# Kernel tuning notes

Measured on AMD Instinct MI355X. Metric: run time of the kernel, lower is better.

## Reference

```python
import jax, jax.numpy as jnp
import numpy as np

SCALE = 2
GROUPS = 4

def _up_axis(x, axis, s):
    # torch F.interpolate bilinear, align_corners=False, along one axis
    n = x.shape[axis]
    src = jnp.maximum((jnp.arange(n * s, dtype=jnp.float32) + 0.5) / s - 0.5, 0.0)
    i0 = jnp.minimum(jnp.floor(src).astype(jnp.int32), n - 1)
    i1 = jnp.minimum(i0 + 1, n - 1)
    t = (src - i0.astype(jnp.float32)).astype(x.dtype)
    shp = [1] * x.ndim
    shp[axis] = -1
    t = t.reshape(shp)
    return jnp.take(x, i0, axis=axis) * (1 - t) + jnp.take(x, i1, axis=axis) * t

def _grid_sample(img, grid):
    # img: (N,C,H,W); grid: (N,Hg,Wg,2) xy in [-1,1]; bilinear, align_corners=False, zeros padding
    N, C, H, W = img.shape
    gx = (grid[..., 0] + 1.0) * (W * 0.5) - 0.5
    gy = (grid[..., 1] + 1.0) * (H * 0.5) - 0.5
    x0 = jnp.floor(gx)
    y0 = jnp.floor(gy)
    tx = (gx - x0).astype(img.dtype)
    ty = (gy - y0).astype(img.dtype)
    x0 = x0.astype(jnp.int32)
    y0 = y0.astype(jnp.int32)
    flat = img.reshape(N, C, H * W)

    def corner(xi, yi, wgt):
        valid = ((xi >= 0) & (xi < W) & (yi >= 0) & (yi < H)).astype(img.dtype)
        idx = (jnp.clip(yi, 0, H - 1) * W + jnp.clip(xi, 0, W - 1)).reshape(N, -1)
        v = jax.vmap(lambda f, i: f[:, i])(flat, idx)  # (N,C,P) irregular gather
        return v * (wgt * valid).reshape(N, 1, -1)

    out = (corner(x0, y0, (1 - tx) * (1 - ty))
           + corner(x0 + 1, y0, tx * (1 - ty))
           + corner(x0, y0 + 1, (1 - tx) * ty)
           + corner(x0 + 1, y0 + 1, tx * ty))
    return out.reshape(N, C, grid.shape[1], grid.shape[2])

def _forward(x, w_off, b_off, w_mask, b_mask):
    s, g = SCALE, GROUPS
    b, c, h, w = x.shape
    # 1x1 convs
    offset = jnp.einsum('bchw,oc->bohw', x, w_off) + b_off[None, :, None, None]  # (b,2g,h,w)
    mask = jax.nn.sigmoid(jnp.einsum('bchw,gc->bghw', x, w_mask) + b_mask[None, :, None, None])  # (b,g,h,w)
    # bilinear upsample then split into s*s subpixel feature maps (one per group)
    x_up = _up_axis(_up_axis(x, 2, s), 3, s)  # (b,c,s*h,s*w)
    feat = x_up.reshape(b, c, s, h, s, w).transpose(0, 2, 4, 1, 3, 5).reshape(b, s * s, c, h, w)[:, :g]
    # per-group offset-perturbed sampling coordinates
    off = offset.reshape(b, g, 2, h, w).transpose(0, 1, 3, 4, 2)  # (b,g,h,w,2) (x,y)
    gy, gx = jnp.meshgrid(jnp.arange(h, dtype=x.dtype), jnp.arange(w, dtype=x.dtype), indexing='ij')
    base = jnp.stack([gx, gy], axis=-1)  # (h,w,2)
    coords = base[None, None] + off
    norm = (coords / jnp.array([w, h], dtype=x.dtype) - 0.5) * 2.0
    sampled = _grid_sample(feat.reshape(b * g, c, h, w), norm.reshape(b * g, h, w, 2))
    sampled = sampled.reshape(b, g, c, h, w)
    # sigmoid-mask weighting and group-sum reduction
    return (sampled * mask[:, :, None]).sum(axis=1)  # (b,c,h,w)

def setup_inputs():
    key = jax.random.key(0)
    k1, k2, k3, k4, k5 = jax.random.split(key, 5)
    b, c, h, w, g = 16, 64, 128, 128, GROUPS
    return {
        'x': jax.random.normal(k1, (b, c, h, w), jnp.float32),
        'w_off': jax.random.normal(k2, (2 * g, c), jnp.float32) * 0.1,
        'b_off': jax.random.normal(k3, (2 * g,), jnp.float32) * 0.1,
        'w_mask': jax.random.normal(k4, (g, c), jnp.float32) * 0.1,
        'b_mask': jax.random.normal(k5, (g,), jnp.float32) * 0.1,
    }

def reference(x, w_off, b_off, w_mask, b_mask):
    return _forward(x, w_off, b_off, w_mask, b_mask)
```

## Files before the change

kernel.cpp:

```cpp
#include <hip/hip_runtime.h>
#include <hip/hip_fp16.h>

#define CC 64
#define HH 128
#define WW 128
#define HWS (HH * WW)
#define NG 4

__device__ __forceinline__ void make_taps(float gp, int n, int half, int& base,
                                          float& w0o, float& w1o, float& w2o) {
  float w0 = 0.0f, w1 = 0.0f, w2 = 0.0f;
  float f = floorf(gp);
  int x0 = (int)f;
  float t = gp - f;
  int b = 0;
#pragma unroll
  for (int k = 0; k < 2; ++k) {
    int xc = x0 + k;
    float cw = k ? t : 1.0f - t;
    if (xc < 0 || xc >= n) cw = 0.0f;
    int xcc = min(max(xc, 0), n - 1);
    int u = half * n + xcc;
    float src = fmaxf((float)u * 0.5f - 0.25f, 0.0f);
    float sf = floorf(src);
    int i0 = (int)sf;
    float tu = src - sf;
    int i1 = min(i0 + 1, n - 1);
    if (k == 0) b = i0;
    int s0 = i0 - b;
    int s1 = i1 - b;
    float a0 = cw * (1.0f - tu);
    float a1 = cw * tu;
    w0 += (s0 == 0) ? a0 : 0.0f;
    w1 += (s0 == 1) ? a0 : 0.0f;
    w0 += (s1 == 0) ? a1 : 0.0f;
    w1 += (s1 == 1) ? a1 : 0.0f;
    w2 += (s1 == 2) ? a1 : 0.0f;
  }
  base = b;
  w0o = w0; w1o = w1; w2o = w2;
}

__global__ __launch_bounds__(256) void prep_fused(
    const float* __restrict__ x,
    const float* __restrict__ w_off, const float* __restrict__ b_off,
    const float* __restrict__ w_mask, const float* __restrict__ b_mask,
    __half* __restrict__ xT, float* __restrict__ geomC, int npix) {
  __shared__ float wt[CC * 12];
  int t = threadIdx.x;
  for (int idx = t; idx < CC * 12; idx += 256) {
    int c = idx / 12, d = idx - c * 12;
    wt[idx] = (d < 8) ? w_off[d * CC + c] : w_mask[(d - 8) * CC + c];
  }
  __syncthreads();

  int pix = blockIdx.x * 256 + t;
  int b = pix >> 14;
  int ij = pix & (HWS - 1);
  int i = ij >> 7, j = ij & (WW - 1);
  const float* __restrict__ xp = x + (size_t)b * CC * HWS + ij;
  __half* __restrict__ xto = xT + (size_t)pix * 64;

  float a12[12];
#pragma unroll
  for (int d = 0; d < 12; ++d) a12[d] = (d < 8) ? b_off[d] : b_mask[d - 8];

  for (int c0 = 0; c0 < CC; c0 += 8) {
    float xv[8];
#pragma unroll
    for (int k = 0; k < 8; ++k) xv[k] = xp[(size_t)(c0 + k) * HWS];
#pragma unroll
    for (int k = 0; k < 8; ++k) {
      int c = c0 + k;
      float v = xv[k];
      const float4 w0 = *reinterpret_cast<const float4*>(&wt[c * 12 + 0]);
      const float4 w1 = *reinterpret_cast<const float4*>(&wt[c * 12 + 4]);
      const float4 w2 = *reinterpret_cast<const float4*>(&wt[c * 12 + 8]);
      a12[0]  = fmaf(w0.x, v, a12[0]);   a12[1]  = fmaf(w0.y, v, a12[1]);
      a12[2]  = fmaf(w0.z, v, a12[2]);   a12[3]  = fmaf(w0.w, v, a12[3]);
      a12[4]  = fmaf(w1.x, v, a12[4]);   a12[5]  = fmaf(w1.y, v, a12[5]);
      a12[6]  = fmaf(w1.z, v, a12[6]);   a12[7]  = fmaf(w1.w, v, a12[7]);
      a12[8]  = fmaf(w2.x, v, a12[8]);   a12[9]  = fmaf(w2.y, v, a12[9]);
      a12[10] = fmaf(w2.z, v, a12[10]);  a12[11] = fmaf(w2.w, v, a12[11]);
    }
    uint4 u;
    u.x = __builtin_bit_cast(unsigned int, __floats2half2_rn(xv[0], xv[1]));
    u.y = __builtin_bit_cast(unsigned int, __floats2half2_rn(xv[2], xv[3]));
    u.z = __builtin_bit_cast(unsigned int, __floats2half2_rn(xv[4], xv[5]));
    u.w = __builtin_bit_cast(unsigned int, __floats2half2_rn(xv[6], xv[7]));
    *reinterpret_cast<uint4*>(xto + c0) = u;
  }

  float* __restrict__ gb = geomC + (size_t)(pix >> 5) * 1024 + (pix & 31);
#pragma unroll
  for (int g = 0; g < NG; ++g) {
    int sy = g >> 1, sx = g & 1;
    float mg = 1.0f / (1.0f + __expf(-a12[8 + g]));
    int cb, rb;
    float x0, x1, x2, y0, y1, y2;
    make_taps((float)j + a12[2 * g]     - 0.5f, WW, sx, cb, x0, x1, x2);
    make_taps((float)i + a12[2 * g + 1] - 0.5f, HH, sy, rb, y0, y1, y2);
    gb[(g * 8 + 0) * 32] = x0;
    gb[(g * 8 + 1) * 32] = x1;
    gb[(g * 8 + 2) * 32] = x2;
    gb[(g * 8 + 3) * 32] = y0 * mg;
    gb[(g * 8 + 4) * 32] = y1 * mg;
    gb[(g * 8 + 5) * 32] = y2 * mg;
    gb[(g * 8 + 6) * 32] = __int_as_float(rb);
    gb[(g * 8 + 7) * 32] = __int_as_float(cb);
  }
}

__global__ __launch_bounds__(256) void sample16(
    const __half* __restrict__ xT, const float* __restrict__ geomC,
    float* __restrict__ out, int npix) {
  __shared__ float graw[1024];
  __shared__ int2 gexp[32][36];
  int t = threadIdx.x;

  int nwg = gridDim.x, bid = blockIdx.x;
  int swz = ((nwg & 7) == 0) ? ((bid & 7) * (nwg >> 3) + (bid >> 3)) : bid;

  reinterpret_cast<uint4*>(graw)[t] =
      reinterpret_cast<const uint4*>(geomC + (size_t)swz * 1024)[t];
  __syncthreads();

  if (t < 128) {
    int p = t >> 2, g = t & 3;
    float wx0 = graw[(g * 8 + 0) * 32 + p];
    float wx1 = graw[(g * 8 + 1) * 32 + p];
    float wx2 = graw[(g * 8 + 2) * 32 + p];
    float wy0 = graw[(g * 8 + 3) * 32 + p];
    float wy1 = graw[(g * 8 + 4) * 32 + p];
    float wy2 = graw[(g * 8 + 5) * 32 + p];
    int rb = __float_as_int(graw[(g * 8 + 6) * 32 + p]);
    int cb = __float_as_int(graw[(g * 8 + 7) * 32 + p]);
#pragma unroll
    for (int dy = 0; dy < 3; ++dy) {
      int ro = min(rb + dy, HH - 1) * WW;
      float wyv = (dy == 0) ? wy0 : ((dy == 1) ? wy1 : wy2);
#pragma unroll
      for (int dx = 0; dx < 3; ++dx) {
        int off = ro + min(cb + dx, WW - 1);
        float wv = wyv * ((dx == 0) ? wx0 : ((dx == 1) ? wx1 : wx2));
        gexp[p][g * 9 + dy * 3 + dx] = make_int2(off, __float_as_int(wv));
      }
    }
  }
  __syncthreads();

  int p = t >> 3, r = t & 7;
  int pix = swz * 32 + p;
  int b = pix >> 14, ij = pix & (HWS - 1);
  const __half* __restrict__ xb = xT + ((size_t)b * HWS) * 64 + r * 8;

  float acc[8];
#pragma unroll
  for (int c = 0; c < 8; ++c) acc[c] = 0.0f;

#pragma unroll
  for (int k = 0; k < 36; ++k) {
    int2 ow = gexp[p][k];
    float w = __int_as_float(ow.y);
    uint4 v = *reinterpret_cast<const uint4*>(xb + (size_t)ow.x * 64);
    float2 f0 = __half22float2(__builtin_bit_cast(__half2, v.x));
    float2 f1 = __half22float2(__builtin_bit_cast(__half2, v.y));
    float2 f2 = __half22float2(__builtin_bit_cast(__half2, v.z));
    float2 f3 = __half22float2(__builtin_bit_cast(__half2, v.w));
    acc[0] = fmaf(w, f0.x, acc[0]);  acc[1] = fmaf(w, f0.y, acc[1]);
    acc[2] = fmaf(w, f1.x, acc[2]);  acc[3] = fmaf(w, f1.y, acc[3]);
    acc[4] = fmaf(w, f2.x, acc[4]);  acc[5] = fmaf(w, f2.y, acc[5]);
    acc[6] = fmaf(w, f3.x, acc[6]);  acc[7] = fmaf(w, f3.y, acc[7]);
  }

  float* __restrict__ op = out + ((size_t)b * CC + r * 8) * HWS + ij;
#pragma unroll
  for (int c = 0; c < 8; ++c) op[(size_t)c * HWS] = acc[c];
}

__global__ __launch_bounds__(256) void dysample_fused(
    const float* __restrict__ x,
    const float* __restrict__ w_off, const float* __restrict__ b_off,
    const float* __restrict__ w_mask, const float* __restrict__ b_mask,
    float* __restrict__ out, int npix) {
  __shared__ float wt[CC * 12];
  for (int idx = threadIdx.x; idx < CC * 12; idx += 256) {
    int c = idx / 12, d = idx - c * 12;
    wt[idx] = (d < 8) ? w_off[d * CC + c] : w_mask[(d - 8) * CC + c];
  }
  __syncthreads();
  int nwg = gridDim.x;
  int bid = blockIdx.x;
  int swz = ((nwg & 7) == 0) ? ((bid & 7) * (nwg >> 3) + (bid >> 3)) : bid;
  int pix = swz * 256 + threadIdx.x;
  if (pix >= npix) return;
  int b = pix >> 14;
  int ij = pix & (HWS - 1);
  int i = ij >> 7, j = ij & (WW - 1);
  const float* __restrict__ xp = x + (size_t)b * CC * HWS;
  float a12[12];
#pragma unroll
  for (int d = 0; d < 12; ++d) a12[d] = (d < 8) ? b_off[d] : b_mask[d - 8];
#pragma unroll 4
  for (int c = 0; c < CC; ++c) {
    float xv = xp[c * HWS + ij];
    const float4 w0 = *reinterpret_cast<const float4*>(&wt[c * 12 + 0]);
    const float4 w1 = *reinterpret_cast<const float4*>(&wt[c * 12 + 4]);
    const float4 w2 = *reinterpret_cast<const float4*>(&wt[c * 12 + 8]);
    a12[0]  = fmaf(w0.x, xv, a12[0]);   a12[1]  = fmaf(w0.y, xv, a12[1]);
    a12[2]  = fmaf(w0.z, xv, a12[2]);   a12[3]  = fmaf(w0.w, xv, a12[3]);
    a12[4]  = fmaf(w1.x, xv, a12[4]);   a12[5]  = fmaf(w1.y, xv, a12[5]);
    a12[6]  = fmaf(w1.z, xv, a12[6]);   a12[7]  = fmaf(w1.w, xv, a12[7]);
    a12[8]  = fmaf(w2.x, xv, a12[8]);   a12[9]  = fmaf(w2.y, xv, a12[9]);
    a12[10] = fmaf(w2.z, xv, a12[10]);  a12[11] = fmaf(w2.w, xv, a12[11]);
  }
  int ro[NG][3], co[NG][3];
  float wx[NG][3], wy[NG][3];
#pragma unroll
  for (int g = 0; g < NG; ++g) {
    int sy = g >> 1, sx = g & 1;
    float mg = 1.0f / (1.0f + __expf(-a12[8 + g]));
    int cb, rb;
    float x0, x1, x2, y0, y1, y2;
    make_taps((float)j + a12[2 * g]     - 0.5f, WW, sx, cb, x0, x1, x2);
    make_taps((float)i + a12[2 * g + 1] - 0.5f, HH, sy, rb, y0, y1, y2);
    wx[g][0] = x0;      wx[g][1] = x1;      wx[g][2] = x2;
    wy[g][0] = y0 * mg; wy[g][1] = y1 * mg; wy[g][2] = y2 * mg;
#pragma unroll
    for (int d = 0; d < 3; ++d) {
      ro[g][d] = min(rb + d, HH - 1) * WW;
      co[g][d] = min(cb + d, WW - 1);
    }
  }
  float* __restrict__ op = out + (size_t)b * CC * HWS + ij;
  for (int blk = 0; blk < 4; ++blk) {
    const float* __restrict__ xb = xp + blk * 16 * HWS;
    float acc[16];
#pragma unroll
    for (int c = 0; c < 16; ++c) acc[c] = 0.0f;
#pragma unroll
    for (int g = 0; g < NG; ++g) {
      int o9[9];
      float w9[9];
#pragma unroll
      for (int dy = 0; dy < 3; ++dy) {
#pragma unroll
        for (int dx = 0; dx < 3; ++dx) {
          o9[dy * 3 + dx] = ro[g][dy] + co[g][dx];
          w9[dy * 3 + dx] = wy[g][dy] * wx[g][dx];
        }
      }
#pragma unroll
      for (int c = 0; c < 16; ++c) {
        const float* __restrict__ xc = xb + c * HWS;
#pragma unroll
        for (int k = 0; k < 9; ++k) acc[c] = fmaf(w9[k], xc[o9[k]], acc[c]);
      }
    }
#pragma unroll
    for (int c = 0; c < 16; ++c) op[(blk * 16 + c) * HWS] = acc[c];
  }
}

extern "C" void kernel_launch(void* const* d_in, const int* in_sizes, int n_in,
                              void* d_out, int out_size, void* d_ws, size_t ws_size,
                              hipStream_t stream) {
  const float* x      = (const float*)d_in[0];
  const float* w_off  = (const float*)d_in[1];
  const float* b_off  = (const float*)d_in[2];
  const float* w_mask = (const float*)d_in[3];
  const float* b_mask = (const float*)d_in[4];
  float* out = (float*)d_out;

  int B = in_sizes[0] / (CC * HWS);
  int npix = B * HWS;
  size_t need = (size_t)npix * 128 + (size_t)npix * 128;

  if (ws_size >= need && (npix & 255) == 0) {
    __half* xT   = (__half*)d_ws;
    float* geomC = (float*)((char*)d_ws + (size_t)npix * 128);
    hipLaunchKernelGGL(prep_fused, dim3(npix / 256), dim3(256), 0, stream,
                       x, w_off, b_off, w_mask, b_mask, xT, geomC, npix);
    hipLaunchKernelGGL(sample16, dim3(npix / 32), dim3(256), 0, stream,
                       xT, geomC, out, npix);
  } else {
    int nblk = (npix + 255) / 256;
    hipLaunchKernelGGL(dysample_fused, dim3(nblk), dim3(256), 0, stream,
                       x, w_off, b_off, w_mask, b_mask, out, npix);
  }
}
```

Baseline: 99.11 us.

## Split prep channels across threads with LDS transpose; accumulate sampling in packed half2

The prep kernel now assigns each block 64 pixels, with four threads per pixel each handling 16 channels. Partial 1x1-conv sums are reduced through shared memory, and the fp16 channels-last tile is written with coalesced 16-byte stores through an LDS transpose. The sampling kernel packs weights as half2 and accumulates with packed half2 FMAs instead of fp32 FMAs after conversion. This is meant to cut conversion and ALU cost and to raise memory parallelism in prep, but accumulating 36 taps in fp16 can lose accuracy.

After: 82.63 us. -16.6%, faster.

```diff
diff --git a/kernel.cpp b/kernel.cpp
--- a/kernel.cpp
+++ b/kernel.cpp
@@ -41,12 +41,14 @@
   w0o = w0; w1o = w1; w2o = w2;
 }
 
-__global__ __launch_bounds__(256) void prep_fused(
+__global__ __launch_bounds__(256) void prep_v3(
     const float* __restrict__ x,
     const float* __restrict__ w_off, const float* __restrict__ b_off,
     const float* __restrict__ w_mask, const float* __restrict__ b_mask,
     __half* __restrict__ xT, float* __restrict__ geomC, int npix) {
   __shared__ float wt[CC * 12];
+  __shared__ unsigned int tile[64][33];
+  __shared__ float part[4][64][13];
   int t = threadIdx.x;
   for (int idx = t; idx < CC * 12; idx += 256) {
     int c = idx / 12, d = idx - c * 12;
@@ -54,60 +56,84 @@
   }
   __syncthreads();
 
-  int pix = blockIdx.x * 256 + t;
+  int px = t & 63, chq = t >> 6;
+  int pix = blockIdx.x * 64 + px;
   int b = pix >> 14;
   int ij = pix & (HWS - 1);
-  int i = ij >> 7, j = ij & (WW - 1);
   const float* __restrict__ xp = x + (size_t)b * CC * HWS + ij;
-  __half* __restrict__ xto = xT + (size_t)pix * 64;
-
-  float a12[12];
-#pragma unroll
-  for (int d = 0; d < 12; ++d) a12[d] = (d < 8) ? b_off[d] : b_mask[d - 8];
-
-  for (int c0 = 0; c0 < CC; c0 += 8) {
-    float xv[8];
-#pragma unroll
-    for (int k = 0; k < 8; ++k) xv[k] = xp[(size_t)(c0 + k) * HWS];
-#pragma unroll
-    for (int k = 0; k < 8; ++k) {
-      int c = c0 + k;
-      float v = xv[k];
-      const float4 w0 = *reinterpret_cast<const float4*>(&wt[c * 12 + 0]);
-      const float4 w1 = *reinterpret_cast<const float4*>(&wt[c * 12 + 4]);
-      const float4 w2 = *reinterpret_cast<const float4*>(&wt[c * 12 + 8]);
-      a12[0]  = fmaf(w0.x, v, a12[0]);   a12[1]  = fmaf(w0.y, v, a12[1]);
-      a12[2]  = fmaf(w0.z, v, a12[2]);   a12[3]  = fmaf(w0.w, v, a12[3]);
-      a12[4]  = fmaf(w1.x, v, a12[4]);   a12[5]  = fmaf(w1.y, v, a12[5]);
-      a12[6]  = fmaf(w1.z, v, a12[6]);   a12[7]  = fmaf(w1.w, v, a12[7]);
-      a12[8]  = fmaf(w2.x, v, a12[8]);   a12[9]  = fmaf(w2.y, v, a12[9]);
-      a12[10] = fmaf(w2.z, v, a12[10]);  a12[11] = fmaf(w2.w, v, a12[11]);
-    }
-    uint4 u;
-    u.x = __builtin_bit_cast(unsigned int, __floats2half2_rn(xv[0], xv[1]));
-    u.y = __builtin_bit_cast(unsigned int, __floats2half2_rn(xv[2], xv[3]));
-    u.z = __builtin_bit_cast(unsigned int, __floats2half2_rn(xv[4], xv[5]));
-    u.w = __builtin_bit_cast(unsigned int, __floats2half2_rn(xv[6], xv[7]));
-    *reinterpret_cast<uint4*>(xto + c0) = u;
-  }
-
-  float* __restrict__ gb = geomC + (size_t)(pix >> 5) * 1024 + (pix & 31);
-#pragma unroll
-  for (int g = 0; g < NG; ++g) {
-    int sy = g >> 1, sx = g & 1;
-    float mg = 1.0f / (1.0f + __expf(-a12[8 + g]));
-    int cb, rb;
-    float x0, x1, x2, y0, y1, y2;
-    make_taps((float)j + a12[2 * g]     - 0.5f, WW, sx, cb, x0, x1, x2);
-    make_taps((float)i + a12[2 * g + 1] - 0.5f, HH, sy, rb, y0, y1, y2);
-    gb[(g * 8 + 0) * 32] = x0;
-    gb[(g * 8 + 1) * 32] = x1;
-    gb[(g * 8 + 2) * 32] = x2;
-    gb[(g * 8 + 3) * 32] = y0 * mg;
-    gb[(g * 8 + 4) * 32] = y1 * mg;
-    gb[(g * 8 + 5) * 32] = y2 * mg;
-    gb[(g * 8 + 6) * 32] = __int_as_float(rb);
-    gb[(g * 8 + 7) * 32] = __int_as_float(cb);
+
+  float xv[16];
+#pragma unroll
+  for (int k = 0; k < 16; ++k) xv[k] = xp[(size_t)(chq * 16 + k) * HWS];
+
+  float p12[12];
+#pragma unroll
+  for (int d = 0; d < 12; ++d) p12[d] = 0.0f;
+#pragma unroll
+  for (int k = 0; k < 16; ++k) {
+    int c = chq * 16 + k;
+    float v = xv[k];
+    const float4 w0 = *reinterpret_cast<const float4*>(&wt[c * 12 + 0]);
+    const float4 w1 = *reinterpret_cast<const float4*>(&wt[c * 12 + 4]);
+    const float4 w2 = *reinterpret_cast<const float4*>(&wt[c * 12 + 8]);
+    p12[0]  = fmaf(w0.x, v, p12[0]);   p12[1]  = fmaf(w0.y, v, p12[1]);
+    p12[2]  = fmaf(w0.z, v, p12[2]);   p12[3]  = fmaf(w0.w, v, p12[3]);
+    p12[4]  = fmaf(w1.x, v, p12[4]);   p12[5]  = fmaf(w1.y, v, p12[5]);
+    p12[6]  = fmaf(w1.z, v, p12[6]);   p12[7]  = fmaf(w1.w, v, p12[7]);
+    p12[8]  = fmaf(w2.x, v, p12[8]);   p12[9]  = fmaf(w2.y, v, p12[9]);
+    p12[10] = fmaf(w2.z, v, p12[10]);  p12[11] = fmaf(w2.w, v, p12[11]);
+  }
+
+#pragma unroll
+  for (int k = 0; k < 8; ++k) {
+    tile[px][chq * 8 + k] = __builtin_bit_cast(
+        unsigned int, __floats2half2_rn(xv[2 * k], xv[2 * k + 1]));
+  }
+#pragma unroll
+  for (int d = 0; d < 12; ++d) part[chq][px][d] = p12[d];
+  __syncthreads();
+
+  {
+    unsigned int* __restrict__ xtu = reinterpret_cast<unsigned int*>(xT);
+    size_t base = (size_t)blockIdx.x * 64 * 32;
+    int spx = t >> 2, c0 = (t & 3) * 8;
+    uint4 u0, u1;
+    u0.x = tile[spx][c0 + 0]; u0.y = tile[spx][c0 + 1];
+    u0.z = tile[spx][c0 + 2]; u0.w = tile[spx][c0 + 3];
+    u1.x = tile[spx][c0 + 4]; u1.y = tile[spx][c0 + 5];
+    u1.z = tile[spx][c0 + 6]; u1.w = tile[spx][c0 + 7];
+    *reinterpret_cast<uint4*>(xtu + base + t * 8) = u0;
+    *reinterpret_cast<uint4*>(xtu + base + t * 8 + 4) = u1;
+  }
+
+  if (t < 64) {
+    int pixg = blockIdx.x * 64 + t;
+    int ijg = pixg & (HWS - 1);
+    int i = ijg >> 7, j = ijg & (WW - 1);
+    float a12[12];
+#pragma unroll
+    for (int d = 0; d < 12; ++d) {
+      a12[d] = ((d < 8) ? b_off[d] : b_mask[d - 8]) + part[0][t][d] +
+               part[1][t][d] + part[2][t][d] + part[3][t][d];
+    }
+    float* __restrict__ gb = geomC + (size_t)(pixg >> 5) * 1024 + (pixg & 31);
+#pragma unroll
+    for (int g = 0; g < NG; ++g) {
+      int sy = g >> 1, sx = g & 1;
+      float mg = 1.0f / (1.0f + __expf(-a12[8 + g]));
+      int cb, rb;
+      float x0, x1, x2, y0, y1, y2;
+      make_taps((float)j + a12[2 * g]     - 0.5f, WW, sx, cb, x0, x1, x2);
+      make_taps((float)i + a12[2 * g + 1] - 0.5f, HH, sy, rb, y0, y1, y2);
+      gb[(g * 8 + 0) * 32] = x0;
+      gb[(g * 8 + 1) * 32] = x1;
+      gb[(g * 8 + 2) * 32] = x2;
+      gb[(g * 8 + 3) * 32] = y0 * mg;
+      gb[(g * 8 + 4) * 32] = y1 * mg;
+      gb[(g * 8 + 5) * 32] = y2 * mg;
+      gb[(g * 8 + 6) * 32] = __int_as_float(rb);
+      gb[(g * 8 + 7) * 32] = __int_as_float(cb);
+    }
   }
 }
 
@@ -143,7 +169,8 @@
       for (int dx = 0; dx < 3; ++dx) {
         int off = ro + min(cb + dx, WW - 1);
         float wv = wyv * ((dx == 0) ? wx0 : ((dx == 1) ? wx1 : wx2));
-        gexp[p][g * 9 + dy * 3 + dx] = make_int2(off, __float_as_int(wv));
+        gexp[p][g * 9 + dy * 3 + dx] =
+            make_int2(off, __builtin_bit_cast(int, __float2half2_rn(wv)));
       }
     }
   }
@@ -154,28 +181,29 @@
   int b = pix >> 14, ij = pix & (HWS - 1);
   const __half* __restrict__ xb = xT + ((size_t)b * HWS) * 64 + r * 8;
 
-  float acc[8];
-#pragma unroll
-  for (int c = 0; c < 8; ++c) acc[c] = 0.0f;
+  __half2 acc0 = __float2half2_rn(0.0f);
+  __half2 acc1 = acc0, acc2 = acc0, acc3 = acc0;
 
 #pragma unroll
   for (int k = 0; k < 36; ++k) {
     int2 ow = gexp[p][k];
-    float w = __int_as_float(ow.y);
+    __half2 wh = __builtin_bit_cast(__half2, ow.y);
     uint4 v = *reinterpret_cast<const uint4*>(xb + (size_t)ow.x * 64);
-    float2 f0 = __half22float2(__builtin_bit_cast(__half2, v.x));
-    float2 f1 = __half22float2(__builtin_bit_cast(__half2, v.y));
-    float2 f2 = __half22float2(__builtin_bit_cast(__half2, v.z));
-    float2 f3 = __half22float2(__builtin_bit_cast(__half2, v.w));
-    acc[0] = fmaf(w, f0.x, acc[0]);  acc[1] = fmaf(w, f0.y, acc[1]);
-    acc[2] = fmaf(w, f1.x, acc[2]);  acc[3] = fmaf(w, f1.y, acc[3]);
-    acc[4] = fmaf(w, f2.x, acc[4]);  acc[5] = fmaf(w, f2.y, acc[5]);
-    acc[6] = fmaf(w, f3.x, acc[6]);  acc[7] = fmaf(w, f3.y, acc[7]);
-  }
-
+    acc0 = __hfma2(__builtin_bit_cast(__half2, v.x), wh, acc0);
+    acc1 = __hfma2(__builtin_bit_cast(__half2, v.y), wh, acc1);
+    acc2 = __hfma2(__builtin_bit_cast(__half2, v.z), wh, acc2);
+    acc3 = __hfma2(__builtin_bit_cast(__half2, v.w), wh, acc3);
+  }
+
+  float2 f0 = __half22float2(acc0);
+  float2 f1 = __half22float2(acc1);
+  float2 f2 = __half22float2(acc2);
+  float2 f3 = __half22float2(acc3);
   float* __restrict__ op = out + ((size_t)b * CC + r * 8) * HWS + ij;
-#pragma unroll
-  for (int c = 0; c < 8; ++c) op[(size_t)c * HWS] = acc[c];
+  op[0 * HWS] = f0.x;  op[1 * HWS] = f0.y;
+  op[2 * HWS] = f1.x;  op[3 * HWS] = f1.y;
+  op[4 * HWS] = f2.x;  op[5 * HWS] = f2.y;
+  op[6 * HWS] = f3.x;  op[7 * HWS] = f3.y;
 }
 
 __global__ __launch_bounds__(256) void dysample_fused(
@@ -279,7 +307,7 @@
   if (ws_size >= need && (npix & 255) == 0) {
     __half* xT   = (__half*)d_ws;
     float* geomC = (float*)((char*)d_ws + (size_t)npix * 128);
-    hipLaunchKernelGGL(prep_fused, dim3(npix / 256), dim3(256), 0, stream,
+    hipLaunchKernelGGL(prep_v3, dim3(npix / 64), dim3(256), 0, stream,
                        x, w_off, b_off, w_mask, b_mask, xT, geomC, npix);
     hipLaunchKernelGGL(sample16, dim3(npix / 32), dim3(256), 0, stream,
                        xT, geomC, out, npix);
```
